# Performance work log

Hardware: AMD Instinct MI355X
Metric: run time of the kernel (lower is better)

Reference implementation:

```python
import jax, jax.numpy as jnp
import numpy as np

N = 50000      # nodes
E = 800000     # edges (avg degree 16)
G = 8          # graphs in batch
D = 128        # in/hidden feats
C = 10         # classes


def setup_inputs() -> dict:
    key = jax.random.key(0)
    ks = jax.random.split(key, 9)
    x = jax.random.normal(ks[0], (N, D), dtype=jnp.float32)
    edge_index = jax.random.randint(ks[1], (2, E), 0, N)
    node2graph = jnp.sort(jax.random.randint(ks[2], (N,), 0, G))
    s = 1.0 / np.sqrt(D)
    W1 = jax.random.normal(ks[3], (D, D), dtype=jnp.float32) * s
    b1 = jnp.zeros((D,), jnp.float32)
    W2 = jax.random.normal(ks[4], (D, D), dtype=jnp.float32) * s
    b2 = jnp.zeros((D,), jnp.float32)
    Wl = jax.random.normal(ks[5], (D, C), dtype=jnp.float32) * s
    bl = jnp.zeros((C,), jnp.float32)
    return {"x": x, "edge_index": edge_index, "node2graph": node2graph,
            "W1": W1, "b1": b1, "W2": W2, "b2": b2, "Wl": Wl, "bl": bl}


def _graph_conv(h, src, dst, out_isqrt, in_isqrt, W, b):
    # DGL GraphConv, norm='both': D_in^{-1/2} A D_out^{-1/2} (h W) + b
    h = (h * out_isqrt[:, None]) @ W
    agg = jax.ops.segment_sum(h[src], dst, num_segments=N)  # SpMM gather/scatter
    return agg * in_isqrt[:, None] + b


def reference(x, edge_index, node2graph, W1, b1, W2, b2, Wl, bl):
    src, dst = edge_index[0], edge_index[1]
    ones_e = jnp.ones((E,), jnp.float32)
    out_deg = jnp.clip(jax.ops.segment_sum(ones_e, src, num_segments=N), 1.0)
    in_deg = jnp.clip(jax.ops.segment_sum(ones_e, dst, num_segments=N), 1.0)
    out_isqrt = jax.lax.rsqrt(out_deg)
    in_isqrt = jax.lax.rsqrt(in_deg)

    h = jax.nn.relu(_graph_conv(x, src, dst, out_isqrt, in_isqrt, W1, b1))
    h = jax.nn.relu(_graph_conv(h, src, dst, out_isqrt, in_isqrt, W2, b2))

    # AvgPooling: per-graph mean of node features
    sums = jax.ops.segment_sum(h, node2graph, num_segments=G)
    counts = jnp.clip(jax.ops.segment_sum(jnp.ones((N,), jnp.float32), node2graph, num_segments=G), 1.0)
    hg = sums / counts[:, None]

    logits = hg @ Wl + bl
    return jax.nn.softmax(logits, axis=1)
```

## Files before the change

kernel.cpp:

```cpp
#include <hip/hip_runtime.h>
#include <stdint.h>

#define FD 128
#define NG 8
#define NC 10
#define MAXB 1024
#define CHUNK 4096

typedef __attribute__((ext_vector_type(8))) short bf16x8;
typedef __attribute__((ext_vector_type(4))) float f32x4;
typedef __attribute__((ext_vector_type(2))) float f32x2;

__device__ __forceinline__ float bf2f(uint16_t u){
    union { uint32_t i; float f; } v; v.i = ((uint32_t)u) << 16; return v.f;
}
__device__ __forceinline__ uint16_t f2bf(float f){
    union { float f; uint32_t i; } v; v.f = f;
    uint32_t r = v.i + 0x7fff + ((v.i >> 16) & 1);
    return (uint16_t)(r >> 16);
}

#if __has_builtin(__builtin_amdgcn_cvt_pk_f32_fp8) && __has_builtin(__builtin_amdgcn_cvt_pk_fp8_f32)
__device__ __forceinline__ f32x2 fp8lo2f(uint32_t p){
    return __builtin_amdgcn_cvt_pk_f32_fp8((int)p, false);
}
__device__ __forceinline__ f32x2 fp8hi2f(uint32_t p){
    return __builtin_amdgcn_cvt_pk_f32_fp8((int)p, true);
}
__device__ __forceinline__ uint32_t pk4fp8(float a, float b, float c, float d){
    int u = 0;
    u = __builtin_amdgcn_cvt_pk_fp8_f32(a, b, u, false);
    u = __builtin_amdgcn_cvt_pk_fp8_f32(c, d, u, true);
    return (uint32_t)u;
}
#else
__device__ __forceinline__ float fp8tof(uint32_t b){
    union { uint32_t i; float f; } v;
    v.i = ((b & 0x7f) << 20) | ((b & 0x80) << 24);
    return v.f * 0x1p120f;
}
__device__ __forceinline__ f32x2 fp8lo2f(uint32_t p){
    return (f32x2){fp8tof(p & 0xff), fp8tof((p >> 8) & 0xff)};
}
__device__ __forceinline__ f32x2 fp8hi2f(uint32_t p){
    return (f32x2){fp8tof((p >> 16) & 0xff), fp8tof((p >> 24) & 0xff)};
}
__device__ __forceinline__ uint32_t f2fp8(float f){
    union { float f; uint32_t i; } v; v.f = f;
    uint32_t s = (v.i >> 24) & 0x80;
    float a = fabsf(f);
    if (a < 0x1p-10f) return s;
    if (a > 448.f) return s | 0x7e;
    v.f = a;
    uint32_t r = v.i + 0x7ffff + ((v.i >> 20) & 1);
    int e = (int)(r >> 23) - 127 + 7;
    uint32_t m = (r >> 20) & 7;
    if (e <= 0){
        uint32_t q = (uint32_t)(a * 512.f + 0.5f);
        return s | (q > 7 ? 8 : q);
    }
    if (e > 15) return s | 0x7e;
    return s | ((uint32_t)e << 3) | m;
}
__device__ __forceinline__ uint32_t pk4fp8(float a, float b, float c, float d){
    return (uint32_t)f2fp8(a) | ((uint32_t)f2fp8(b)<<8) |
           ((uint32_t)f2fp8(c)<<16) | ((uint32_t)f2fp8(d)<<24);
}
#endif

__global__ __launch_bounds__(256) void k_prep(const float* __restrict__ W1,
        const float* __restrict__ W2, uint16_t* Wf1, uint16_t* Wf2,
        const int* __restrict__ ei, int E, int B, int C, int shift,
        int* __restrict__ cnt, float* __restrict__ pool,
        unsigned long long* __restrict__ state, int* __restrict__ counters){
    int t = threadIdx.x;
    if (blockIdx.x < 128){
        int id = blockIdx.x*256 + t;
        int w = id >> 14;
        int r = id & 16383;
        int j = r & 7, frag = r >> 3;
        int lane = frag & 63, t2 = frag >> 6;
        int n = t2 & 7, kk = t2 >> 3;
        int k = kk*32 + (lane>>4)*8 + j;
        int col = n*16 + (lane&15);
        float v = (w ? W2 : W1)[k*128 + col];
        (w ? Wf2 : Wf1)[r] = f2bf(v);
        if (blockIdx.x == 0){
            for (int i = t; i < NG*FD; i += 256) pool[i] = 0.f;
            for (int i = t; i < 1024; i += 256) state[i] = 0ull;
            if (t < 8) counters[t] = 0;
        }
        return;
    }
    __shared__ int hd[MAXB], hs[MAXB];
    int c = blockIdx.x - 128;
    for (int i=t;i<B;i+=256){ hd[i]=0; hs[i]=0; }
    __syncthreads();
    int e0 = c*CHUNK, e1 = min(E, e0+CHUNK);
    for (int e = e0+t; e < e1; e += 256){
        int s = ei[e], d = ei[E+e];
        atomicAdd(&hd[d>>shift], 1);
        atomicAdd(&hs[s>>shift], 1);
    }
    __syncthreads();
    for (int i=t;i<B;i+=256){
        cnt[(size_t)i*C + c]     = hd[i];
        cnt[(size_t)(B+i)*C + c] = hs[i];
    }
}

#define SEPT 16
#define STILE 4096
__global__ __launch_bounds__(256) void k_scan(int* __restrict__ a, int M,
        unsigned long long* __restrict__ state, int* __restrict__ ticket){
    __shared__ int bid_s, exc_s;
    __shared__ int s[256];
    int t = threadIdx.x;
    if (t == 0) bid_s = atomicAdd(ticket, 1);
    __syncthreads();
    int bid = bid_s;
    int base = bid*STILE + t*SEPT;
    int v[SEPT]; int sum = 0;
    #pragma unroll
    for (int i=0;i<SEPT;i++){ int idx=base+i; int x=(idx<M)?a[idx]:0; v[i]=sum; sum+=x; }
    s[t]=sum; __syncthreads();
    for (int o=1;o<256;o<<=1){ int x=(t>=o)?s[t-o]:0; __syncthreads(); s[t]+=x; __syncthreads(); }
    int tot = s[255];
    int te = s[t]-sum;
    if (t == 0){
        unsigned long long pub = ((bid==0) ? (2ull<<62) : (1ull<<62)) | (unsigned long long)(unsigned)tot;
        __hip_atomic_store(&state[bid], pub, __ATOMIC_RELEASE, __HIP_MEMORY_SCOPE_AGENT);
        int exc = 0;
        if (bid > 0){
            int p = bid-1;
            while (true){
                unsigned long long st = __hip_atomic_load(&state[p], __ATOMIC_ACQUIRE, __HIP_MEMORY_SCOPE_AGENT);
                unsigned long long fl = st >> 62;
                if (fl == 2ull){ exc += (int)(unsigned)st; break; }
                if (fl == 1ull){ exc += (int)(unsigned)st; p--; }
            }
            __hip_atomic_store(&state[bid],
                (2ull<<62) | (unsigned long long)(unsigned)(exc + tot),
                __ATOMIC_RELEASE, __HIP_MEMORY_SCOPE_AGENT);
        }
        exc_s = exc;
    }
    __syncthreads();
    int exc = exc_s;
    #pragma unroll
    for (int i=0;i<SEPT;i++){ int idx=base+i; if (idx<M) a[idx]=exc+te+v[i]; }
}

__global__ __launch_bounds__(256) void k_scatter(const int* __restrict__ ei, int E,
        int B, int C, int shift, const int* __restrict__ scan,
        uint32_t* __restrict__ tempD, uint16_t* __restrict__ tempS){
    __shared__ int cd[MAXB], cs[MAXB];
    int t = threadIdx.x, c = blockIdx.x;
    for (int i=t;i<B;i+=256){
        cd[i] = scan[(size_t)i*C + c];
        cs[i] = scan[(size_t)(B+i)*C + c] - E;
    }
    __syncthreads();
    int e0 = c*CHUNK, e1 = min(E, e0+CHUNK);
    int lmask = (1<<shift) - 1;
    for (int e = e0+t; e < e1; e += 256){
        int s = ei[e], d = ei[E+e];
        int p = atomicAdd(&cd[d>>shift], 1);
        tempD[p] = ((uint32_t)(d & lmask) << 20) | (uint32_t)s;
        int q = atomicAdd(&cs[s>>shift], 1);
        tempS[q] = (uint16_t)s;
    }
}

__global__ __launch_bounds__(256) void k_build2(const uint32_t* __restrict__ tempD,
        const uint16_t* __restrict__ tempS, const int* __restrict__ scan,
        int B, int C, int shift, int E, int N,
        int* __restrict__ row_off, int* __restrict__ csr, int* __restrict__ deg_out){
    __shared__ int cnt[MAXB];
    __shared__ int offl[MAXB];
    int b = blockIdx.x, t = threadIdx.x;
    int range = 1<<shift, nb0 = b<<shift;
    int seg0 = scan[(size_t)b*C];
    int seg1 = (b+1<B) ? scan[(size_t)(b+1)*C] : E;
    for (int i=t;i<range;i+=256) cnt[i]=0;
    __syncthreads();
    for (int i=seg0+t; i<seg1; i+=256)
        atomicAdd(&cnt[tempD[i]>>20], 1);
    __syncthreads();
    if (t==0){ int run=0; for (int i=0;i<range;i++){ offl[i]=run; run+=cnt[i]; } }
    __syncthreads();
    for (int i=t;i<range;i+=256){
        int node = nb0+i;
        if (node < N) row_off[node] = seg0 + offl[i];
    }
    if (b==B-1 && t==0) row_off[N] = E;
    for (int i=t;i<range;i+=256) cnt[i] = offl[i];
    __syncthreads();
    for (int i=seg0+t; i<seg1; i+=256){
        uint32_t v = tempD[i];
        int p = atomicAdd(&cnt[v>>20], 1);
        csr[seg0 + p] = (int)(v & 0xFFFFFu);
    }
    __syncthreads();
    int sg0 = scan[(size_t)(B+b)*C] - E;
    int sg1 = ((b+1<B) ? scan[(size_t)(B+b+1)*C] : 2*E) - E;
    for (int i=t;i<range;i+=256) cnt[i]=0;
    __syncthreads();
    for (int i=sg0+t; i<sg1; i+=256)
        atomicAdd(&cnt[(int)tempS[i] - nb0], 1);
    __syncthreads();
    for (int i=t;i<range;i+=256){
        int node = nb0+i;
        if (node < N) deg_out[node] = cnt[i];
    }
}

__global__ __launch_bounds__(256) void k_gemm(const void* __restrict__ A,
        const uint16_t* __restrict__ Wf, const int* __restrict__ deg_out,
        uint8_t* __restrict__ out8, int nrows, int amode){
    int t = threadIdx.x;
    int wave = t>>6, lane = t&63, quad = lane>>4, low = lane&15;

    int rowA  = blockIdx.x*64 + wave*16 + low;
    int rowAc = min(rowA, nrows-1);

    bf16x8 ah[4];
    if (amode){
        const uint16_t* arow = (const uint16_t*)A + (size_t)rowAc*FD;
        #pragma unroll
        for (int kk=0;kk<4;kk++)
            ah[kk] = *(const bf16x8*)(arow + kk*32 + quad*8);
    } else {
        const float* arow = (const float*)A + (size_t)rowAc*FD;
        #pragma unroll
        for (int kk=0;kk<4;kk++){
            f32x4 f0 = *(const f32x4*)(arow + kk*32 + quad*8);
            f32x4 f1 = *(const f32x4*)(arow + kk*32 + quad*8 + 4);
            #pragma unroll
            for (int j=0;j<4;j++) ah[kk][j]   = (short)f2bf(f0[j]);
            #pragma unroll
            for (int j=0;j<4;j++) ah[kk][j+4] = (short)f2bf(f1[j]);
        }
    }

    f32x4 acc[8];
    #pragma unroll
    for (int n=0;n<8;n++) acc[n] = (f32x4){0.f,0.f,0.f,0.f};

    #pragma unroll
    for (int kk=0;kk<4;kk++){
        #pragma unroll
        for (int n=0;n<8;n++){
            bf16x8 bh = *(const bf16x8*)(Wf + ((size_t)((kk*8+n)*64 + lane))*8);
            acc[n] = __builtin_amdgcn_mfma_f32_16x16x32_bf16(bh, ah[kk], acc[n], 0, 0, 0);
        }
    }

    if (rowA < nrows){
        float sc = rsqrtf((float)max(deg_out[rowA], 1));
        uint8_t* orow = out8 + (size_t)rowA*FD;
        #pragma unroll
        for (int n=0;n<8;n++){
            uint32_t pk = pk4fp8(acc[n][0]*sc, acc[n][1]*sc, acc[n][2]*sc, acc[n][3]*sc);
            *(uint32_t*)(orow + n*16 + quad*4) = pk;
        }
    }
}

__global__ __launch_bounds__(256) void k_spmm(const uint8_t* __restrict__ tmp8,
        const int* __restrict__ row_off, const int* __restrict__ csr_src,
        const float* __restrict__ bias, uint16_t* __restrict__ hout, int N){
    int tid = threadIdx.x;
    int node = blockIdx.x*16 + (tid>>4);
    int l  = tid & 15;
    int qb = (tid & 63) & 48;
    if (node >= N) return;
    int e0 = row_off[node], e1 = row_off[node+1];
    const uint2* tp = (const uint2*)tmp8;
    f32x2 a01={0.f,0.f}, a23={0.f,0.f}, a45={0.f,0.f}, a67={0.f,0.f};
    for (int base = e0; base < e1; base += 16){
        int my = 0;
        if (base + l < e1) my = csr_src[base + l];
        int cnt = min(16, e1 - base);
        for (int j0 = 0; j0 < cnt; j0 += 8){
            int ss[8];
            #pragma unroll
            for (int k=0;k<8;k++)
                ss[k] = __shfl(my, qb + min(j0 + k, cnt-1));
            uint2 p[8];
            #pragma unroll
            for (int k=0;k<8;k++)
                p[k] = tp[(size_t)ss[k]*16 + l];
            #pragma unroll
            for (int k=0;k<8;k++){
                if (j0 + k < cnt){
                    a01 += fp8lo2f(p[k].x); a23 += fp8hi2f(p[k].x);
                    a45 += fp8lo2f(p[k].y); a67 += fp8hi2f(p[k].y);
                }
            }
        }
    }
    float isq = rsqrtf((float)max(e1 - e0, 1));
    f32x4 b0 = *(const f32x4*)(bias + l*8);
    f32x4 b1 = *(const f32x4*)(bias + l*8 + 4);
    float r0 = fmaxf(a01.x*isq + b0[0], 0.f);
    float r1 = fmaxf(a01.y*isq + b0[1], 0.f);
    float r2 = fmaxf(a23.x*isq + b0[2], 0.f);
    float r3 = fmaxf(a23.y*isq + b0[3], 0.f);
    float r4 = fmaxf(a45.x*isq + b1[0], 0.f);
    float r5 = fmaxf(a45.y*isq + b1[1], 0.f);
    float r6 = fmaxf(a67.x*isq + b1[2], 0.f);
    float r7 = fmaxf(a67.y*isq + b1[3], 0.f);
    uint4 o;
    o.x = (uint32_t)f2bf(r0) | ((uint32_t)f2bf(r1) << 16);
    o.y = (uint32_t)f2bf(r2) | ((uint32_t)f2bf(r3) << 16);
    o.z = (uint32_t)f2bf(r4) | ((uint32_t)f2bf(r5) << 16);
    o.w = (uint32_t)f2bf(r6) | ((uint32_t)f2bf(r7) << 16);
    *(uint4*)(hout + (size_t)node*FD + l*8) = o;
}

__global__ __launch_bounds__(256) void k_pool(const uint16_t* __restrict__ h,
        const int* __restrict__ n2g, int N, float* __restrict__ pool){
    __shared__ float sacc[NG*FD];
    int t = threadIdx.x;
    for (int i = t; i < NG*FD; i += 256) sacc[i] = 0.f;
    __syncthreads();
    int fp = t & 63;
    int no = t >> 6;
    const uint32_t* hp = (const uint32_t*)h;
    int base = blockIdx.x * 64;
    int gg[16]; uint32_t pv[16];
    #pragma unroll
    for (int i = 0; i < 16; i++){
        int node = base + i*4 + no;
        int nc = min(node, N-1);
        gg[i] = n2g[nc];
        uint32_t v = hp[(size_t)nc*64 + fp];
        pv[i] = (node < N) ? v : 0u;
    }
    float r0 = 0.f, r1 = 0.f; int rg = gg[0];
    #pragma unroll
    for (int i = 0; i < 16; i++){
        if (gg[i] != rg){
            atomicAdd(&sacc[rg*FD + fp*2],     r0);
            atomicAdd(&sacc[rg*FD + fp*2 + 1], r1);
            r0 = r1 = 0.f; rg = gg[i];
        }
        r0 += bf2f((uint16_t)(pv[i] & 0xffff));
        r1 += bf2f((uint16_t)(pv[i] >> 16));
    }
    atomicAdd(&sacc[rg*FD + fp*2],     r0);
    atomicAdd(&sacc[rg*FD + fp*2 + 1], r1);
    __syncthreads();
    for (int i = t; i < NG*FD; i += 256){
        float v = sacc[i];
        if (v != 0.f) atomicAdd(&pool[i], v);
    }
}

__global__ __launch_bounds__(128) void k_final(const float* __restrict__ pool,
        const int* __restrict__ n2g, int N, const float* __restrict__ Wl,
        const float* __restrict__ bl, float* __restrict__ out){
    __shared__ int ub[NG+1];
    __shared__ float logits[NG][NC];
    int t = threadIdx.x;
    if (t <= NG){
        int lo = 0, hi = N;
        while (lo < hi){ int mid = (lo+hi)>>1; if (n2g[mid] < t) lo = mid+1; else hi = mid; }
        ub[t] = lo;
    }
    __syncthreads();
    if (t < NG*NC){
        int g = t/NC, c = t%NC;
        float cnt = (float)max(ub[g+1]-ub[g], 1);
        float inv = 1.f/cnt;
        float acc = bl[c];
        for (int d=0; d<FD; d++)
            acc += pool[g*FD+d]*inv * Wl[d*NC+c];
        logits[g][c] = acc;
    }
    __syncthreads();
    if (t < NG*NC){
        int g = t/NC, c = t%NC;
        float m = -1e30f;
        for (int i=0;i<NC;i++) m = fmaxf(m, logits[g][i]);
        float ssum = 0.f;
        for (int i=0;i<NC;i++) ssum += expf(logits[g][i]-m);
        out[t] = expf(logits[g][c]-m)/ssum;
    }
}

extern "C" void kernel_launch(void* const* d_in, const int* in_sizes, int n_in,
                              void* d_out, int out_size, void* d_ws, size_t ws_size,
                              hipStream_t stream) {
    const float* x   = (const float*)d_in[0];
    const int*   ei  = (const int*)d_in[1];
    const int*   n2g = (const int*)d_in[2];
    const float* W1  = (const float*)d_in[3];
    const float* b1  = (const float*)d_in[4];
    const float* W2  = (const float*)d_in[5];
    const float* b2  = (const float*)d_in[6];
    const float* Wl  = (const float*)d_in[7];
    const float* bl  = (const float*)d_in[8];
    float* outp = (float*)d_out;

    int N = in_sizes[2];
    int E = in_sizes[1] / 2;

    int shift = 6;
    while ((((N + (1<<shift) - 1) >> shift) > MAXB) && shift < 10) shift++;
    int B = (N + (1<<shift) - 1) >> shift;
    int C = (E + CHUNK - 1) / CHUNK;
    int M = 2*B*C;
    int nscan = (M + STILE - 1) / STILE;

    char* w = (char*)d_ws;
    size_t off = 0;
    auto alloc = [&](size_t bytes)->char*{ char* p = w + off; off += (bytes + 255) & ~(size_t)255; return p; };
    float*    pool    = (float*)alloc((size_t)NG*FD*4);
    unsigned long long* state = (unsigned long long*)alloc(1024*8);
    int*      counters= (int*)alloc(8*4);
    int*      deg_out = (int*)alloc((size_t)N*4);
    int*      row_off = (int*)alloc((size_t)(N+1)*4);
    int*      csr     = (int*)alloc((size_t)E*4);
    uint16_t* Wf1     = (uint16_t*)alloc(16384*2);
    uint16_t* Wf2     = (uint16_t*)alloc(16384*2);
    uint8_t*  tmp8    = (uint8_t*)alloc((size_t)N*FD);
    uint16_t* hb      = (uint16_t*)alloc((size_t)N*FD*2);
    (void)ws_size;
    uint32_t* tempD = (uint32_t*)tmp8;
    uint16_t* tempS = (uint16_t*)(tmp8 + (size_t)E*4);
    int* cnt = (int*)hb;

    k_prep   <<<128 + C, 256, 0, stream>>>(W1, W2, Wf1, Wf2, ei, E, B, C, shift,
                                           cnt, pool, state, counters);
    k_scan   <<<nscan, 256, 0, stream>>>(cnt, M, state, &counters[0]);
    k_scatter<<<C, 256, 0, stream>>>(ei, E, B, C, shift, cnt, tempD, tempS);
    k_build2 <<<B, 256, 0, stream>>>(tempD, tempS, cnt, B, C, shift, E, N, row_off, csr, deg_out);

    int gb = (N + 63)/64;
    int sb = (N + 15)/16;
    int pb = (N + 63)/64;
    k_gemm  <<<gb, 256, 0, stream>>>(x,  Wf1, deg_out, tmp8, N, 0);
    k_spmm  <<<sb, 256, 0, stream>>>(tmp8, row_off, csr, b1, hb, N);
    k_gemm  <<<gb, 256, 0, stream>>>(hb, Wf2, deg_out, tmp8, N, 1);
    k_spmm  <<<sb, 256, 0, stream>>>(tmp8, row_off, csr, b2, hb, N);
    k_pool  <<<pb, 256, 0, stream>>>(hb, n2g, N, pool);
    k_final <<<1,  128, 0, stream>>>(pool, n2g, N, Wl, bl, outp);
}
```

Before: 218.3 us.

## Fuse first SpMM with second GEMM and second SpMM with pooling

Layer-1 aggregation now writes its bf16 rows into shared memory, and the layer-2 MFMA GEMM runs in the same block, producing fp8 output directly. Layer-2 aggregation accumulates per-graph sums in registers and LDS and feeds the pool, so the bf16 hidden buffer is never written or read. This removes two launches and two full N×128 round trips through global memory. In exchange, each block handles 64 rows with four sequential gathers per 16-lane group, which lowers parallelism and latency hiding, and a separate count buffer is now allocated.

```diff
diff --git a/kernel.cpp b/kernel.cpp
--- a/kernel.cpp
+++ b/kernel.cpp
@@ -267,17 +267,9 @@
     }
 }
 
-__global__ __launch_bounds__(256) void k_spmm(const uint8_t* __restrict__ tmp8,
-        const int* __restrict__ row_off, const int* __restrict__ csr_src,
-        const float* __restrict__ bias, uint16_t* __restrict__ hout, int N){
-    int tid = threadIdx.x;
-    int node = blockIdx.x*16 + (tid>>4);
-    int l  = tid & 15;
-    int qb = (tid & 63) & 48;
-    if (node >= N) return;
-    int e0 = row_off[node], e1 = row_off[node+1];
-    const uint2* tp = (const uint2*)tmp8;
-    f32x2 a01={0.f,0.f}, a23={0.f,0.f}, a45={0.f,0.f}, a67={0.f,0.f};
+__device__ __forceinline__ void spmm_row(const uint2* __restrict__ tp,
+        const int* __restrict__ csr_src, int e0, int e1, int l, int qb,
+        f32x2& a01, f32x2& a23, f32x2& a45, f32x2& a67){
     for (int base = e0; base < e1; base += 16){
         int my = 0;
         if (base + l < e1) my = csr_src[base + l];
@@ -300,59 +292,126 @@
             }
         }
     }
-    float isq = rsqrtf((float)max(e1 - e0, 1));
-    f32x4 b0 = *(const f32x4*)(bias + l*8);
-    f32x4 b1 = *(const f32x4*)(bias + l*8 + 4);
-    float r0 = fmaxf(a01.x*isq + b0[0], 0.f);
-    float r1 = fmaxf(a01.y*isq + b0[1], 0.f);
-    float r2 = fmaxf(a23.x*isq + b0[2], 0.f);
-    float r3 = fmaxf(a23.y*isq + b0[3], 0.f);
-    float r4 = fmaxf(a45.x*isq + b1[0], 0.f);
-    float r5 = fmaxf(a45.y*isq + b1[1], 0.f);
-    float r6 = fmaxf(a67.x*isq + b1[2], 0.f);
-    float r7 = fmaxf(a67.y*isq + b1[3], 0.f);
-    uint4 o;
-    o.x = (uint32_t)f2bf(r0) | ((uint32_t)f2bf(r1) << 16);
-    o.y = (uint32_t)f2bf(r2) | ((uint32_t)f2bf(r3) << 16);
-    o.z = (uint32_t)f2bf(r4) | ((uint32_t)f2bf(r5) << 16);
-    o.w = (uint32_t)f2bf(r6) | ((uint32_t)f2bf(r7) << 16);
-    *(uint4*)(hout + (size_t)node*FD + l*8) = o;
-}
-
-__global__ __launch_bounds__(256) void k_pool(const uint16_t* __restrict__ h,
-        const int* __restrict__ n2g, int N, float* __restrict__ pool){
+}
+
+__global__ __launch_bounds__(256) void k_spmm_gemm(const uint8_t* __restrict__ tmp8,
+        const int* __restrict__ row_off, const int* __restrict__ csr_src,
+        const float* __restrict__ bias, const uint16_t* __restrict__ Wf,
+        const int* __restrict__ deg_out, uint8_t* __restrict__ out8, int N){
+    __shared__ __align__(16) uint16_t hsrow[64][136];
+    int tid = threadIdx.x;
+    int l = tid & 15, qid = tid >> 4, qb = (tid & 63) & 48;
+    const uint2* tp = (const uint2*)tmp8;
+    f32x4 bv0 = *(const f32x4*)(bias + l*8);
+    f32x4 bv1 = *(const f32x4*)(bias + l*8 + 4);
+    #pragma unroll
+    for (int i = 0; i < 4; i++){
+        int rowL = qid*4 + i;
+        int node = blockIdx.x*64 + rowL;
+        int e0 = 0, e1 = 0;
+        if (node < N){ e0 = row_off[node]; e1 = row_off[node+1]; }
+        f32x2 a01={0.f,0.f}, a23={0.f,0.f}, a45={0.f,0.f}, a67={0.f,0.f};
+        spmm_row(tp, csr_src, e0, e1, l, qb, a01, a23, a45, a67);
+        float isq = rsqrtf((float)max(e1 - e0, 1));
+        float r0 = fmaxf(a01.x*isq + bv0[0], 0.f);
+        float r1 = fmaxf(a01.y*isq + bv0[1], 0.f);
+        float r2 = fmaxf(a23.x*isq + bv0[2], 0.f);
+        float r3 = fmaxf(a23.y*isq + bv0[3], 0.f);
+        float r4 = fmaxf(a45.x*isq + bv1[0], 0.f);
+        float r5 = fmaxf(a45.y*isq + bv1[1], 0.f);
+        float r6 = fmaxf(a67.x*isq + bv1[2], 0.f);
+        float r7 = fmaxf(a67.y*isq + bv1[3], 0.f);
+        uint4 o;
+        o.x = (uint32_t)f2bf(r0) | ((uint32_t)f2bf(r1) << 16);
+        o.y = (uint32_t)f2bf(r2) | ((uint32_t)f2bf(r3) << 16);
+        o.z = (uint32_t)f2bf(r4) | ((uint32_t)f2bf(r5) << 16);
+        o.w = (uint32_t)f2bf(r6) | ((uint32_t)f2bf(r7) << 16);
+        if (node >= N) o = (uint4){0u,0u,0u,0u};
+        *(uint4*)(&hsrow[rowL][l*8]) = o;
+    }
+    __syncthreads();
+    int wave = tid>>6, lane = tid&63, quad = lane>>4, low = lane&15;
+    int rowL = wave*16 + low;
+    int rowA = blockIdx.x*64 + rowL;
+    bf16x8 ah[4];
+    #pragma unroll
+    for (int kk=0;kk<4;kk++)
+        ah[kk] = *(const bf16x8*)(&hsrow[rowL][kk*32 + quad*8]);
+    f32x4 acc[8];
+    #pragma unroll
+    for (int n=0;n<8;n++) acc[n] = (f32x4){0.f,0.f,0.f,0.f};
+    #pragma unroll
+    for (int kk=0;kk<4;kk++){
+        #pragma unroll
+        for (int n=0;n<8;n++){
+            bf16x8 bh = *(const bf16x8*)(Wf + ((size_t)((kk*8+n)*64 + lane))*8);
+            acc[n] = __builtin_amdgcn_mfma_f32_16x16x32_bf16(bh, ah[kk], acc[n], 0, 0, 0);
+        }
+    }
+    if (rowA < N){
+        float sc = rsqrtf((float)max(deg_out[rowA], 1));
+        uint8_t* orow = out8 + (size_t)rowA*FD;
+        #pragma unroll
+        for (int n=0;n<8;n++){
+            uint32_t pk = pk4fp8(acc[n][0]*sc, acc[n][1]*sc, acc[n][2]*sc, acc[n][3]*sc);
+            *(uint32_t*)(orow + n*16 + quad*4) = pk;
+        }
+    }
+}
+
+__global__ __launch_bounds__(256) void k_spmm_pool(const uint8_t* __restrict__ tmp8,
+        const int* __restrict__ row_off, const int* __restrict__ csr_src,
+        const float* __restrict__ bias, const int* __restrict__ n2g,
+        float* __restrict__ pool, int N){
     __shared__ float sacc[NG*FD];
-    int t = threadIdx.x;
-    for (int i = t; i < NG*FD; i += 256) sacc[i] = 0.f;
-    __syncthreads();
-    int fp = t & 63;
-    int no = t >> 6;
-    const uint32_t* hp = (const uint32_t*)h;
-    int base = blockIdx.x * 64;
-    int gg[16]; uint32_t pv[16];
-    #pragma unroll
-    for (int i = 0; i < 16; i++){
-        int node = base + i*4 + no;
-        int nc = min(node, N-1);
-        gg[i] = n2g[nc];
-        uint32_t v = hp[(size_t)nc*64 + fp];
-        pv[i] = (node < N) ? v : 0u;
-    }
-    float r0 = 0.f, r1 = 0.f; int rg = gg[0];
-    #pragma unroll
-    for (int i = 0; i < 16; i++){
-        if (gg[i] != rg){
-            atomicAdd(&sacc[rg*FD + fp*2],     r0);
-            atomicAdd(&sacc[rg*FD + fp*2 + 1], r1);
-            r0 = r1 = 0.f; rg = gg[i];
-        }
-        r0 += bf2f((uint16_t)(pv[i] & 0xffff));
-        r1 += bf2f((uint16_t)(pv[i] >> 16));
-    }
-    atomicAdd(&sacc[rg*FD + fp*2],     r0);
-    atomicAdd(&sacc[rg*FD + fp*2 + 1], r1);
-    __syncthreads();
-    for (int i = t; i < NG*FD; i += 256){
+    int tid = threadIdx.x;
+    for (int i = tid; i < NG*FD; i += 256) sacc[i] = 0.f;
+    __syncthreads();
+    int l = tid & 15, qid = tid >> 4, qb = (tid & 63) & 48;
+    const uint2* tp = (const uint2*)tmp8;
+    f32x4 bv0 = *(const f32x4*)(bias + l*8);
+    f32x4 bv1 = *(const f32x4*)(bias + l*8 + 4);
+    int rg = -1;
+    float racc[8];
+    #pragma unroll
+    for (int j=0;j<8;j++) racc[j] = 0.f;
+    #pragma unroll
+    for (int i = 0; i < 4; i++){
+        int node = blockIdx.x*64 + qid*4 + i;
+        if (node < N){
+            int e0 = row_off[node], e1 = row_off[node+1];
+            f32x2 a01={0.f,0.f}, a23={0.f,0.f}, a45={0.f,0.f}, a67={0.f,0.f};
+            spmm_row(tp, csr_src, e0, e1, l, qb, a01, a23, a45, a67);
+            float isq = rsqrtf((float)max(e1 - e0, 1));
+            float r[8];
+            r[0] = fmaxf(a01.x*isq + bv0[0], 0.f);
+            r[1] = fmaxf(a01.y*isq + bv0[1], 0.f);
+            r[2] = fmaxf(a23.x*isq + bv0[2], 0.f);
+            r[3] = fmaxf(a23.y*isq + bv0[3], 0.f);
+            r[4] = fmaxf(a45.x*isq + bv1[0], 0.f);
+            r[5] = fmaxf(a45.y*isq + bv1[1], 0.f);
+            r[6] = fmaxf(a67.x*isq + bv1[2], 0.f);
+            r[7] = fmaxf(a67.y*isq + bv1[3], 0.f);
+            int g = n2g[node];
+            if (g != rg){
+                if (rg >= 0){
+                    #pragma unroll
+                    for (int j=0;j<8;j++) atomicAdd(&sacc[rg*FD + l*8 + j], racc[j]);
+                }
+                rg = g;
+                #pragma unroll
+                for (int j=0;j<8;j++) racc[j] = 0.f;
+            }
+            #pragma unroll
+            for (int j=0;j<8;j++) racc[j] += r[j];
+        }
+    }
+    if (rg >= 0){
+        #pragma unroll
+        for (int j=0;j<8;j++) atomicAdd(&sacc[rg*FD + l*8 + j], racc[j]);
+    }
+    __syncthreads();
+    for (int i = tid; i < NG*FD; i += 256){
         float v = sacc[i];
         if (v != 0.f) atomicAdd(&pool[i], v);
     }
@@ -426,11 +485,11 @@
     uint16_t* Wf1     = (uint16_t*)alloc(16384*2);
     uint16_t* Wf2     = (uint16_t*)alloc(16384*2);
     uint8_t*  tmp8    = (uint8_t*)alloc((size_t)N*FD);
-    uint16_t* hb      = (uint16_t*)alloc((size_t)N*FD*2);
+    uint8_t*  tmp8b   = (uint8_t*)alloc((size_t)N*FD);
+    int*      cnt     = (int*)alloc((size_t)M*4);
     (void)ws_size;
     uint32_t* tempD = (uint32_t*)tmp8;
     uint16_t* tempS = (uint16_t*)(tmp8 + (size_t)E*4);
-    int* cnt = (int*)hb;
 
     k_prep   <<<128 + C, 256, 0, stream>>>(W1, W2, Wf1, Wf2, ei, E, B, C, shift,
                                            cnt, pool, state, counters);
@@ -439,12 +498,8 @@
     k_build2 <<<B, 256, 0, stream>>>(tempD, tempS, cnt, B, C, shift, E, N, row_off, csr, deg_out);
 
     int gb = (N + 63)/64;
-    int sb = (N + 15)/16;
-    int pb = (N + 63)/64;
-    k_gemm  <<<gb, 256, 0, stream>>>(x,  Wf1, deg_out, tmp8, N, 0);
-    k_spmm  <<<sb, 256, 0, stream>>>(tmp8, row_off, csr, b1, hb, N);
-    k_gemm  <<<gb, 256, 0, stream>>>(hb, Wf2, deg_out, tmp8, N, 1);
-    k_spmm  <<<sb, 256, 0, stream>>>(tmp8, row_off, csr, b2, hb, N);
-    k_pool  <<<pb, 256, 0, stream>>>(hb, n2g, N, pool);
-    k_final <<<1,  128, 0, stream>>>(pool, n2g, N, Wl, bl, outp);
-}
+    k_gemm      <<<gb, 256, 0, stream>>>(x, Wf1, deg_out, tmp8, N, 0);
+    k_spmm_gemm <<<gb, 256, 0, stream>>>(tmp8,  row_off, csr, b1, Wf2, deg_out, tmp8b, N);
+    k_spmm_pool <<<gb, 256, 0, stream>>>(tmp8b, row_off, csr, b2, n2g, pool, N);
+    k_final     <<<1,  128, 0, stream>>>(pool, n2g, N, Wl, bl, outp);
+}
```

Measured after the change: 223.3 us. 2.3% more time.
